# Kernel tuning notes

Hardware: AMD Instinct MI355X
Metric: run time of the kernel (lower is better)

Reference implementation:

```python
import jax, jax.numpy as jnp
import numpy as np

TAU = 0.5
EPS = 1e-6
RAY_STEPS = 128
N_SECANT = 8
STEPS_IN = 64
STEPS_OUT = 32
RADIUS = 1.0
ADA_START, ADA_END, ADA_DECAY = 2.0, 0.1, 1.5e-5
IT = 100000
DEPTH_NEAR = 0.0
DELTA = float(max(ADA_START * np.exp(-ADA_DECAY * IT), ADA_END))


def _occ_val(p, W1, b1, W2, b2):
    # occupancy probability minus tau (sign change = surface crossing)
    h = jax.nn.softplus(p @ W1 + b1)
    return jax.nn.sigmoid((h @ W2 + b2)[..., 0]) - TAU


def _rgb_alpha(p, v, W1, b1, W2, b2, Wc1, bc1, Wc2, bc2):
    alpha = _occ_val(p, W1, b1, W2, b2) + TAU
    f = jax.nn.relu(jnp.concatenate([p, v], -1) @ Wc1 + bc1)
    rgb = jax.nn.sigmoid(f @ Wc2 + bc2)
    return rgb, alpha


def _forward(pixels, camera_mat, world_mat, scale_mat, W1, b1, W2, b2, Wc1, bc1, Wc2, bc2):
    B, N, _ = pixels.shape
    # transform_to_world with all matrices inverted: p_world = S^-1 W^-1 C^-1 p_hom
    M = jnp.linalg.inv(scale_mat) @ jnp.linalg.inv(world_mat) @ jnp.linalg.inv(camera_mat)
    ones = jnp.ones((B, N, 1), pixels.dtype)
    p_h = jnp.concatenate([pixels, ones, ones], -1)  # (x, y, 1, 1) with depth 1
    pixels_world = jnp.einsum('bij,bnj->bni', M, p_h)[..., :3]
    origin = jnp.array([0.0, 0.0, 0.0, 1.0], pixels.dtype)
    cam0 = jnp.einsum('bij,j->bi', M, origin)[..., :3]                 # (B,3)
    camera_world = jnp.broadcast_to(cam0[:, None, :], (B, N, 3))
    ray = pixels_world - camera_world
    ray = ray / jnp.linalg.norm(ray, axis=-1, keepdims=True)

    # ---- sphere intersection ----
    rcd = jnp.einsum('bnd,bd->bn', ray, cam0)
    under = rcd ** 2 - (jnp.sum(cam0 ** 2, -1)[:, None] - RADIUS ** 2)
    mask_int = under > 0
    s = jnp.sqrt(jnp.where(mask_int, under, 1.0))                      # safe sqrt
    inters = jnp.stack([-s - rcd, s - rcd], -1)
    inters = jnp.where(mask_int[..., None], inters, 0.0)
    inters = jnp.maximum(inters, 0.0)                                  # (B,N,2)
    d_far = inters[..., 1]

    # ---- ray marching + secant root finding (no grad in original) ----
    t = jnp.linspace(0.0, 1.0, RAY_STEPS, dtype=pixels.dtype)
    d_prop = d_far[..., None] * t                                      # (B,N,S)
    p_prop = camera_world[:, :, None, :] + ray[:, :, None, :] * d_prop[..., None]
    val = _occ_val(p_prop, W1, b1, W2, b2)                             # (B,N,S)
    mask_0_free = val[..., 0] < 0
    sign = jnp.sign(val[..., :-1] * val[..., 1:])
    sign = jnp.concatenate([sign, jnp.ones_like(sign[..., :1])], -1)
    cost = sign * jnp.arange(RAY_STEPS, 0, -1, dtype=pixels.dtype)
    ind = jnp.argmin(cost, -1)
    mask_sc = jnp.min(cost, -1) < 0
    f_low = jnp.take_along_axis(val, ind[..., None], -1)[..., 0]
    mask = mask_sc & (f_low < 0) & mask_int & mask_0_free
    ind_hi = jnp.minimum(ind + 1, RAY_STEPS - 1)
    d_low = jnp.take_along_axis(d_prop, ind[..., None], -1)[..., 0]
    d_high = jnp.take_along_axis(d_prop, ind_hi[..., None], -1)[..., 0]
    f_high = jnp.take_along_axis(val, ind_hi[..., None], -1)[..., 0]

    def sec(f_l, f_h, d_l, d_h):
        den = f_h - f_l
        return jnp.where(jnp.abs(den) > 1e-12, -f_l * (d_h - d_l) / den + d_l, 0.5 * (d_l + d_h))

    def body(i, c):
        d_p, d_l, f_l, d_h, f_h = c
        f_m = _occ_val(camera_world + ray * d_p[..., None], W1, b1, W2, b2)
        low = f_m < 0
        d_l = jnp.where(low, d_p, d_l); f_l = jnp.where(low, f_m, f_l)
        d_h = jnp.where(low, d_h, d_p); f_h = jnp.where(low, f_h, f_m)
        return (sec(f_l, f_h, d_l, d_h), d_l, f_l, d_h, f_h)

    d_pred0 = sec(f_low, f_high, d_low, d_high)
    d_pred, _, _, _, _ = jax.lax.fori_loop(0, N_SECANT, body, (d_pred0, d_low, f_low, d_high, f_high))
    d_i = jnp.where(mask, d_pred, jnp.inf)
    d_i = jnp.where(mask_0_free, d_i, 0.0)
    d_i = jax.lax.stop_gradient(d_i)

    # ---- depth interval selection ----
    mask_zero = d_i == 0
    mask_pred = jnp.isfinite(d_i)
    dists = jnp.where(mask_pred, d_i, 1.0)
    dists = jnp.where(mask_zero, 0.0, dists)[0]                        # batch 1, as original
    obj_mask = (mask_pred & ~mask_zero)[0]                             # (N,)
    cam_f = camera_world.reshape(-1, 3)
    ray_f = ray.reshape(-1, 3)
    d_surf = inters.reshape(-1, 2)[:, 1]
    dnp = jnp.maximum(dists - DELTA, DEPTH_NEAR)
    dfp = jnp.minimum(dists + DELTA, d_surf)
    FULL = STEPS_IN + STEPS_OUT
    t_full = jnp.linspace(0.0, 1.0, FULL, dtype=pixels.dtype)
    d_bg = d_surf[:, None] * t_full                                    # depth_range[0] = 0
    t_in = jnp.linspace(0.0, 1.0, STEPS_IN, dtype=pixels.dtype)
    t_out = jnp.linspace(0.0, 1.0, STEPS_OUT, dtype=pixels.dtype)
    d_in = dnp[:, None] * (1.0 - t_in) + dfp[:, None] * t_in
    d_out = dnp[:, None] * t_out
    d_obj = jnp.sort(jnp.concatenate([d_out, d_in], -1), -1)
    d_all = jnp.where(obj_mask[:, None], d_obj, d_bg)                  # (N, FULL)

    # ---- shading + alpha compositing ----
    p_fg = cam_f[:, None, :] + ray_f[:, None, :] * d_all[..., None]    # (N,FULL,3)
    v_fg = jnp.broadcast_to(-ray_f[:, None, :], p_fg.shape)
    rgb, alpha = _rgb_alpha(p_fg, v_fg, W1, b1, W2, b2, Wc1, bc1, Wc2, bc2)
    trans = jnp.cumprod(jnp.concatenate([jnp.ones_like(alpha[:, :1]), 1.0 - alpha + EPS], -1), -1)[:, :-1]
    w = alpha * trans
    rgb_values = jnp.sum(w[..., None] * rgb, -2)
    return rgb_values.reshape(B, N, 3)


def setup_inputs() -> dict:
    key = jax.random.key(0)
    ks = jax.random.split(key, 8)
    B, N, H = 1, 4096, 128
    pixels = jax.random.uniform(ks[0], (B, N, 2), minval=-1.0, maxval=1.0, dtype=jnp.float32)
    camera_mat = jnp.broadcast_to(jnp.diag(jnp.array([2.0, 2.0, 1.0, 1.0], jnp.float32)), (B, 4, 4))
    world_mat = jnp.broadcast_to(jnp.array([[1, 0, 0, 0], [0, 1, 0, 0], [0, 0, 1, 2.0], [0, 0, 0, 1]], jnp.float32), (B, 4, 4))
    scale_mat = jnp.broadcast_to(jnp.eye(4, dtype=jnp.float32), (B, 4, 4))
    W1 = jax.random.normal(ks[1], (3, H), jnp.float32)
    b1 = 0.1 * jax.random.normal(ks[2], (H,), jnp.float32)
    W2 = 0.5 * jax.random.normal(ks[3], (H, 1), jnp.float32)
    b2 = jnp.zeros((1,), jnp.float32)
    Wc1 = 0.5 * jax.random.normal(ks[4], (6, H), jnp.float32)
    bc1 = jnp.zeros((H,), jnp.float32)
    Wc2 = 0.5 * jax.random.normal(ks[5], (H, 3), jnp.float32)
    bc2 = jnp.zeros((3,), jnp.float32)
    return dict(pixels=pixels, camera_mat=camera_mat, world_mat=world_mat, scale_mat=scale_mat,
                W1=W1, b1=b1, W2=W2, b2=b2, Wc1=Wc1, bc1=bc1, Wc2=Wc2, bc2=bc2)


def reference(pixels, camera_mat, world_mat, scale_mat, W1, b1, W2, b2, Wc1, bc1, Wc2, bc2):
    return _forward(pixels, camera_mat, world_mat, scale_mat, W1, b1, W2, b2, Wc1, bc1, Wc2, bc2)
```

## Files before the change

kernel.cpp:

```cpp
#include <hip/hip_runtime.h>
#include <math.h>


namespace {

constexpr int H_    = 128;
constexpr int RS    = 128;
constexpr int NSEC  = 8;
constexpr int SOUT_ = 32;
constexpr int SIN_  = 64;
constexpr int FULL_ = 96;
constexpr int RPB   = 4;
constexpr float EPSA   = 1e-6f;
constexpr float DELTA_ = 0.44626032029685964f;
constexpr float L2E    = 1.4426950408889634f;
constexpr float LN2    = 0.6931471805599453f;

typedef __attribute__((ext_vector_type(2))) float f2;

__device__ __forceinline__ f2 s2(float v) { return f2{v, v}; }

constexpr float PC0 =  0.5849625007211562f;
constexpr float PC1 =  0.4808983469629878f;
constexpr float PC2 = -0.0801497244938313f;
constexpr float PC3 =  0.0178110498875181f;
constexpr float PC4 = -0.0044527624718795f;
constexpr float PC5 =  0.0011873633258345f;
constexpr float PC6 = -0.0003298231460651f;

__device__ __forceinline__ f2 sp2p(f2 u) {
    f2 e;
    e.x = __builtin_amdgcn_exp2f(-fabsf(u.x));
    e.y = __builtin_amdgcn_exp2f(-fabsf(u.y));
    f2 t = e + e - 1.0f;
    f2 p = s2(PC6);
    p = __builtin_elementwise_fma(p, t, s2(PC5));
    p = __builtin_elementwise_fma(p, t, s2(PC4));
    p = __builtin_elementwise_fma(p, t, s2(PC3));
    p = __builtin_elementwise_fma(p, t, s2(PC2));
    p = __builtin_elementwise_fma(p, t, s2(PC1));
    p = __builtin_elementwise_fma(p, t, s2(PC0));
    return __builtin_elementwise_max(u, s2(0.0f)) + p;
}

__device__ __forceinline__ float sigmoid_fast(float x) {
    return __builtin_amdgcn_rcpf(1.0f + __expf(-x));
}
__device__ __forceinline__ float sgnf(float p) {
    return (p > 0.0f) ? 1.0f : ((p < 0.0f) ? -1.0f : 0.0f);
}
__device__ __forceinline__ float secant_step(float f_l, float f_h, float d_l, float d_h) {
    float den = f_h - f_l;
    if (fabsf(den) > 1e-12f) return -f_l * (d_h - d_l) / den + d_l;
    return 0.5f * (d_l + d_h);
}
__device__ __forceinline__ float2 ld2(const float* p) {
    return *reinterpret_cast<const float2*>(p);
}

__device__ void inv4(const float* m, float* o) {
    float inv[16];
    inv[0]  =  m[5]*m[10]*m[15] - m[5]*m[11]*m[14] - m[9]*m[6]*m[15] + m[9]*m[7]*m[14] + m[13]*m[6]*m[11] - m[13]*m[7]*m[10];
    inv[4]  = -m[4]*m[10]*m[15] + m[4]*m[11]*m[14] + m[8]*m[6]*m[15] - m[8]*m[7]*m[14] - m[12]*m[6]*m[11] + m[12]*m[7]*m[10];
    inv[8]  =  m[4]*m[9]*m[15]  - m[4]*m[11]*m[13] - m[8]*m[5]*m[15] + m[8]*m[7]*m[13] + m[12]*m[5]*m[11] - m[12]*m[7]*m[9];
    inv[12] = -m[4]*m[9]*m[14]  + m[4]*m[10]*m[13] + m[8]*m[5]*m[14] - m[8]*m[6]*m[13] - m[12]*m[5]*m[10] + m[12]*m[6]*m[9];
    inv[1]  = -m[1]*m[10]*m[15] + m[1]*m[11]*m[14] + m[9]*m[2]*m[15] - m[9]*m[3]*m[14] - m[13]*m[2]*m[11] + m[13]*m[3]*m[10];
    inv[5]  =  m[0]*m[10]*m[15] - m[0]*m[11]*m[14] - m[8]*m[2]*m[15] + m[8]*m[3]*m[14] + m[12]*m[2]*m[11] - m[12]*m[3]*m[10];
    inv[9]  = -m[0]*m[9]*m[15]  + m[0]*m[11]*m[13] + m[8]*m[1]*m[15] - m[8]*m[3]*m[13] - m[12]*m[1]*m[11] + m[12]*m[3]*m[9];
    inv[13] =  m[0]*m[9]*m[14]  - m[0]*m[10]*m[13] - m[8]*m[1]*m[14] + m[8]*m[2]*m[13] + m[12]*m[1]*m[10] - m[12]*m[2]*m[9];
    inv[2]  =  m[1]*m[6]*m[15]  - m[1]*m[7]*m[14]  - m[5]*m[2]*m[15] + m[5]*m[3]*m[14] + m[13]*m[2]*m[7]  - m[13]*m[3]*m[6];
    inv[6]  = -m[0]*m[6]*m[15]  + m[0]*m[7]*m[14]  + m[4]*m[2]*m[15] - m[4]*m[3]*m[14] - m[12]*m[2]*m[7]  + m[12]*m[3]*m[6];
    inv[10] =  m[0]*m[5]*m[15]  - m[0]*m[7]*m[13]  - m[4]*m[1]*m[15] + m[4]*m[3]*m[13] + m[12]*m[1]*m[7]  - m[12]*m[3]*m[5];
    inv[14] = -m[0]*m[5]*m[14]  + m[0]*m[6]*m[13]  + m[4]*m[1]*m[14] - m[4]*m[2]*m[13] - m[12]*m[1]*m[6]  + m[12]*m[2]*m[5];
    inv[3]  = -m[1]*m[6]*m[11]  + m[1]*m[7]*m[10]  + m[5]*m[2]*m[11] - m[5]*m[3]*m[10] - m[9]*m[2]*m[7]   + m[9]*m[3]*m[6];
    inv[7]  =  m[0]*m[6]*m[11]  - m[0]*m[7]*m[10]  - m[4]*m[2]*m[11] + m[4]*m[3]*m[10] + m[8]*m[2]*m[7]   - m[8]*m[3]*m[6];
    inv[11] = -m[0]*m[5]*m[11]  + m[0]*m[7]*m[9]   + m[4]*m[1]*m[11] - m[4]*m[3]*m[9]  - m[8]*m[1]*m[7]   + m[8]*m[3]*m[5];
    inv[15] =  m[0]*m[5]*m[10]  - m[0]*m[6]*m[9]   - m[4]*m[1]*m[10] + m[4]*m[2]*m[9]  + m[8]*m[1]*m[6]   - m[8]*m[2]*m[5];
    float det = m[0]*inv[0] + m[1]*inv[4] + m[2]*inv[8] + m[3]*inv[12];
    float idet = 1.0f / det;
    for (int i = 0; i < 16; i++) o[i] = inv[i] * idet;
}

__global__ __launch_bounds__(64 * RPB) void render_k(
    const float* __restrict__ pixels,
    const float* __restrict__ Cm, const float* __restrict__ Wm, const float* __restrict__ Sm,
    const float* __restrict__ W1, const float* __restrict__ b1,
    const float* __restrict__ W2, const float* __restrict__ b2,
    const float* __restrict__ Wc1, const float* __restrict__ bc1,
    const float* __restrict__ Wc2, const float* __restrict__ bc2,
    float* __restrict__ out, int N)
{
    const int tid  = threadIdx.x;
    const int lane = tid & 63;
    const int wid  = tid >> 6;
    const int r    = blockIdx.x * RPB + wid;
    const int rr   = (r < N) ? r : (N - 1);

    __shared__ float4 sP0[RPB][H_/2];
    __shared__ float4 sP1[RPB][H_/2];
    __shared__ float4 sP2[RPB][H_/2];
    __shared__ float4 sP3[RPB][H_/2];
    __shared__ f2     sW2[RPB][H_/2];
    __shared__ float  sInv[3][16];
    __shared__ float  sT[16], sM[16];

    const int u0 = 2 * lane;
    const float2 w1xv = ld2(W1 + u0);
    const float2 w1yv = ld2(W1 + H_ + u0);
    const float2 w1zv = ld2(W1 + 2*H_ + u0);
    const float2 b1v  = ld2(b1 + u0);
    const float2 w2v  = ld2(W2 + u0);
    const float2 q0v  = ld2(Wc1 + u0);
    const float2 q1v  = ld2(Wc1 + H_ + u0);
    const float2 q2v  = ld2(Wc1 + 2*H_ + u0);
    const float2 q3v  = ld2(Wc1 + 3*H_ + u0);
    const float2 q4v  = ld2(Wc1 + 4*H_ + u0);
    const float2 q5v  = ld2(Wc1 + 5*H_ + u0);
    const float2 bc1v = ld2(bc1 + u0);
    const float2 wc2a = ld2(Wc2 + 3*u0);
    const float2 wc2b = ld2(Wc2 + 3*u0 + 2);
    const float2 wc2c = ld2(Wc2 + 3*u0 + 4);
    const float b2v  = b2[0];
    const float bc20 = bc2[0], bc21 = bc2[1], bc22 = bc2[2];

    if (wid == 0) {
        const float* mm = (lane == 0) ? Cm : ((lane == 1) ? Wm : Sm);
        float o[16];
        inv4(mm, o);
        if (lane < 3)
            for (int k = 0; k < 16; k++) sInv[lane][k] = o[k];
    }
    __syncthreads();
    if (wid == 0 && lane < 16) {
        int row = lane >> 2, col = lane & 3;
        float s = 0.0f;
        for (int k = 0; k < 4; k++) s += sInv[1][row*4 + k] * sInv[0][k*4 + col];
        sT[lane] = s;
    }
    __syncthreads();
    if (wid == 0 && lane < 16) {
        int row = lane >> 2, col = lane & 3;
        float s = 0.0f;
        for (int k = 0; k < 4; k++) s += sInv[2][row*4 + k] * sT[k*4 + col];
        sM[lane] = s;
    }
    __syncthreads();

    float cx, cy, cz, rx, ry, rz, dfar;
    int mint;
    {
        const float px_ = pixels[2*rr], py_ = pixels[2*rr + 1];
        float cam[3], dir[3];
        for (int i = 0; i < 3; i++) {
            cam[i] = sM[4*i + 3];
            float pw = sM[4*i + 0]*px_ + sM[4*i + 1]*py_ + sM[4*i + 2] + sM[4*i + 3];
            dir[i] = pw - cam[i];
        }
        float nrm = sqrtf(dir[0]*dir[0] + dir[1]*dir[1] + dir[2]*dir[2]);
        rx = dir[0]/nrm; ry = dir[1]/nrm; rz = dir[2]/nrm;
        cx = cam[0]; cy = cam[1]; cz = cam[2];
        float rcd = rx*cx + ry*cy + rz*cz;
        float cc  = cx*cx + cy*cy + cz*cz;
        float under = rcd*rcd - (cc - 1.0f);
        mint = under > 0.0f;
        float s = sqrtf(mint ? under : 1.0f);
        dfar = mint ? fmaxf(s - rcd, 0.0f) : 0.0f;
    }

    float a2k[2], c2k[2], w2k[2];
    float cCr[2], w0r[2], w1r[2], w2r[2];
    {
        a2k[0] = (w1xv.x*rx + w1yv.x*ry + w1zv.x*rz) * L2E;
        a2k[1] = (w1xv.y*rx + w1yv.y*ry + w1zv.y*rz) * L2E;
        c2k[0] = (w1xv.x*cx + w1yv.x*cy + w1zv.x*cz + b1v.x) * L2E;
        c2k[1] = (w1xv.y*cx + w1yv.y*cy + w1zv.y*cz + b1v.y) * L2E;
        w2k[0] = w2v.x * LN2;
        w2k[1] = w2v.y * LN2;
        float aC0 = q0v.x*rx + q1v.x*ry + q2v.x*rz;
        float aC1 = q0v.y*rx + q1v.y*ry + q2v.y*rz;
        cCr[0] = q0v.x*cx + q1v.x*cy + q2v.x*cz + bc1v.x - (q3v.x*rx + q4v.x*ry + q5v.x*rz);
        cCr[1] = q0v.y*cx + q1v.y*cy + q2v.y*cz + bc1v.y - (q3v.y*rx + q4v.y*ry + q5v.y*rz);
        w0r[0] = wc2a.x; w1r[0] = wc2a.y; w2r[0] = wc2b.x;
        w0r[1] = wc2b.y; w1r[1] = wc2c.x; w2r[1] = wc2c.y;
        sP0[wid][lane] = float4{a2k[0], a2k[1], c2k[0], c2k[1]};
        sP1[wid][lane] = float4{w2k[0], w2k[1], aC0, aC1};
        sP2[wid][lane] = float4{cCr[0], cCr[1], w0r[0], w0r[1]};
        sP3[wid][lane] = float4{w1r[0], w1r[1], w2r[0], w2r[1]};
        sW2[wid][lane] = f2{w2k[0], w2k[1]};
    }
    __syncthreads();

    float alpha0, r0c, g0c, b0c;
    float alpha1, r1c, g1c, b1c;

    if (dfar == 0.0f) {
        f2 sp = sp2p(f2{c2k[0], c2k[1]});
        float part = sp.x*w2k[0] + sp.y*w2k[1];
        f2 ff = __builtin_elementwise_max(f2{cCr[0], cCr[1]}, s2(0.0f));
        float A0 = ff.x*w0r[0] + ff.y*w0r[1];
        float A1 = ff.x*w1r[0] + ff.y*w1r[1];
        float A2 = ff.x*w2r[0] + ff.y*w2r[1];
#pragma unroll
        for (int off = 32; off; off >>= 1) {
            part += __shfl_xor(part, off, 64);
            A0   += __shfl_xor(A0,   off, 64);
            A1   += __shfl_xor(A1,   off, 64);
            A2   += __shfl_xor(A2,   off, 64);
        }
        alpha0 = sigmoid_fast(part + b2v);
        r0c = sigmoid_fast(A0 + bc20);
        g0c = sigmoid_fast(A1 + bc21);
        b0c = sigmoid_fast(A2 + bc22);
        alpha1 = alpha0; r1c = r0c; g1c = g0c; b1c = b0c;
    } else {
        const float inv127 = 1.0f / (RS - 1);

        float l0;
        {
            f2 sp = sp2p(f2{c2k[0], c2k[1]});
            float part = sp.x*w2k[0] + sp.y*w2k[1];
#pragma unroll
            for (int off = 32; off; off >>= 1) part += __shfl_xor(part, off, 64);
            l0 = part + b2v;
        }

        float d_i;
        if (l0 >= 0.0f) {
            d_i = 0.0f;
        } else {
            auto march_logit = [&](float dsmp) -> float {
                const f2 dd = s2(dsmp);
                f2 acc = s2(0.0f);
#pragma unroll 4
                for (int j2 = 0; j2 < H_/2; j2++) {
                    float4 q0 = sP0[wid][j2];
                    f2 wv = sW2[wid][j2];
                    f2 u = __builtin_elementwise_fma(f2{q0.x, q0.y}, dd, f2{q0.z, q0.w});
                    acc = __builtin_elementwise_fma(sp2p(u), wv, acc);
                }
                return acc.x + acc.y + b2v;
            };

            float lA = march_logit(dfar * ((float)lane * inv127));
            float va = sigmoid_fast(lA) - 0.5f;
            float van = __shfl_down(va, 1, 64);
            float ca = (lane < 63) ? sgnf(va * van) * (float)(RS - lane) : 1.0f;
            float cmin = ca; int ind = lane;
#pragma unroll
            for (int off = 32; off; off >>= 1) {
                float c2 = __shfl_xor(cmin, off, 64);
                int   i2 = __shfl_xor(ind,  off, 64);
                if (c2 < cmin || (c2 == cmin && i2 < ind)) { cmin = c2; ind = i2; }
            }
            int crossed = cmin < 0.0f;
            float f_low = 0.0f, f_high = 0.0f;
            if (crossed) {
                f_low  = __shfl(va, ind, 64);
                f_high = __shfl(va, ind + 1, 64);
            } else {
                float lB = march_logit(dfar * ((float)(lane + 64) * inv127));
                float vb = sigmoid_fast(lB) - 0.5f;
                float v63 = __shfl(va, 63, 64);
                float v64 = __shfl(vb, 0, 64);
                if (v63 * v64 < 0.0f) {
                    crossed = 1; ind = 63;
                    f_low = v63; f_high = v64;
                } else {
                    float vbn = __shfl_down(vb, 1, 64);
                    float cb = (lane < 63) ? sgnf(vb * vbn) * (float)(64 - lane) : 1.0f;
                    float cminb = cb; int indl = lane;
#pragma unroll
                    for (int off = 32; off; off >>= 1) {
                        float c2 = __shfl_xor(cminb, off, 64);
                        int   i2 = __shfl_xor(indl,  off, 64);
                        if (c2 < cminb || (c2 == cminb && i2 < indl)) { cminb = c2; indl = i2; }
                    }
                    if (cminb < 0.0f) {
                        crossed = 1; ind = 64 + indl;
                        f_low  = __shfl(vb, indl, 64);
                        f_high = __shfl(vb, indl + 1, 64);
                    }
                }
            }

            const int msk = crossed && (f_low < 0.0f) && mint;
            if (msk) {
                float d_l = dfar * ((float)ind * inv127);
                float d_h = dfar * ((float)(ind + 1) * inv127);
                float f_l = f_low, f_h = f_high;
                float d_p = secant_step(f_l, f_h, d_l, d_h);
                for (int it = 0; it < NSEC; it++) {
                    f2 u2 = __builtin_elementwise_fma(f2{a2k[0], a2k[1]}, s2(d_p),
                                                      f2{c2k[0], c2k[1]});
                    f2 sp = sp2p(u2);
                    float part = sp.x*w2k[0] + sp.y*w2k[1];
#pragma unroll
                    for (int off = 32; off; off >>= 1) part += __shfl_xor(part, off, 64);
                    float fm = sigmoid_fast(part + b2v) - 0.5f;
                    bool low = fm < 0.0f;
                    d_l = low ? d_p : d_l;  f_l = low ? fm : f_l;
                    d_h = low ? d_h : d_p;  f_h = low ? f_h : fm;
                    d_p = secant_step(f_l, f_h, d_l, d_h);
                }
                d_i = d_p;
            } else {
                d_i = INFINITY;
            }
        }

        const int mask_zero = (d_i == 0.0f);
        const int mask_pred = isfinite(d_i);
        float dists = mask_pred ? d_i : 1.0f;
        if (mask_zero) dists = 0.0f;
        const int obj = mask_pred && !mask_zero;
        const float dnp = fmaxf(dists - DELTA_, 0.0f);
        const float dfp = fminf(dists + DELTA_, dfar);

        auto sample_d = [&](int s) -> float {
            if (obj) {
                if (s < SOUT_) return dnp * ((float)s * (1.0f / (SOUT_ - 1)));
                float u = (float)(s - SOUT_) * (1.0f / (SIN_ - 1));
                return dnp * (1.0f - u) + dfp * u;
            }
            return dfar * ((float)s * (1.0f / (FULL_ - 1)));
        };

        {
            const f2 dd = s2(sample_d(lane));
            f2 SO = s2(0.0f), A0 = s2(0.0f), A1 = s2(0.0f), A2 = s2(0.0f);
#pragma unroll 4
            for (int j2 = 0; j2 < H_/2; j2++) {
                float4 q0 = sP0[wid][j2];
                float4 q1 = sP1[wid][j2];
                float4 q2 = sP2[wid][j2];
                float4 q3 = sP3[wid][j2];
                f2 u = __builtin_elementwise_fma(f2{q0.x, q0.y}, dd, f2{q0.z, q0.w});
                SO = __builtin_elementwise_fma(sp2p(u), f2{q1.x, q1.y}, SO);
                f2 f = __builtin_elementwise_max(
                           __builtin_elementwise_fma(f2{q1.z, q1.w}, dd, f2{q2.x, q2.y}),
                           s2(0.0f));
                A0 = __builtin_elementwise_fma(f, f2{q2.z, q2.w}, A0);
                A1 = __builtin_elementwise_fma(f, f2{q3.x, q3.y}, A1);
                A2 = __builtin_elementwise_fma(f, f2{q3.z, q3.w}, A2);
            }
            alpha0 = sigmoid_fast(SO.x + SO.y + b2v);
            r0c = sigmoid_fast(A0.x + A0.y + bc20);
            g0c = sigmoid_fast(A1.x + A1.y + bc21);
            b0c = sigmoid_fast(A2.x + A2.y + bc22);
        }

        {
            const int s1 = 64 + (lane & 31);
            const int jb = (lane >> 5) * (H_/4);
            const f2 dd = s2(sample_d(s1));
            f2 SO = s2(0.0f), A0 = s2(0.0f), A1 = s2(0.0f), A2 = s2(0.0f);
#pragma unroll 4
            for (int j2 = jb; j2 < jb + H_/4; j2++) {
                float4 q0 = sP0[wid][j2];
                float4 q1 = sP1[wid][j2];
                float4 q2 = sP2[wid][j2];
                float4 q3 = sP3[wid][j2];
                f2 u = __builtin_elementwise_fma(f2{q0.x, q0.y}, dd, f2{q0.z, q0.w});
                SO = __builtin_elementwise_fma(sp2p(u), f2{q1.x, q1.y}, SO);
                f2 f = __builtin_elementwise_max(
                           __builtin_elementwise_fma(f2{q1.z, q1.w}, dd, f2{q2.x, q2.y}),
                           s2(0.0f));
                A0 = __builtin_elementwise_fma(f, f2{q2.z, q2.w}, A0);
                A1 = __builtin_elementwise_fma(f, f2{q3.x, q3.y}, A1);
                A2 = __builtin_elementwise_fma(f, f2{q3.z, q3.w}, A2);
            }
            float SOs = SO.x + SO.y, A0s = A0.x + A0.y;
            float A1s = A1.x + A1.y, A2s = A2.x + A2.y;
            SOs += __shfl_xor(SOs, 32, 64);
            A0s += __shfl_xor(A0s, 32, 64);
            A1s += __shfl_xor(A1s, 32, 64);
            A2s += __shfl_xor(A2s, 32, 64);
            alpha1 = sigmoid_fast(SOs + b2v);
            r1c = sigmoid_fast(A0s + bc20);
            g1c = sigmoid_fast(A1s + bc21);
            b1c = sigmoid_fast(A2s + bc22);
        }
    }

    {
        float mA = 1.0f - alpha0 + EPSA;
        float p = mA;
#pragma unroll
        for (int off = 1; off < 64; off <<= 1) {
            float v = __shfl_up(p, off, 64);
            if (lane >= off) p *= v;
        }
        float TexA = __shfl_up(p, 1, 64);
        if (lane == 0) TexA = 1.0f;
        float TA = __shfl(p, 63, 64);
        float wA = alpha0 * TexA;

        float mB = (lane < 32) ? (1.0f - alpha1 + EPSA) : 1.0f;
        float pb = mB;
#pragma unroll
        for (int off = 1; off < 32; off <<= 1) {
            float v = __shfl_up(pb, off, 64);
            if (lane >= off) pb *= v;
        }
        float TexB = __shfl_up(pb, 1, 64);
        if (lane == 0) TexB = 1.0f;
        float wB = (lane < 32) ? alpha1 * TexB * TA : 0.0f;

        float s0 = wA*r0c + wB*r1c;
        float s1 = wA*g0c + wB*g1c;
        float s2v = wA*b0c + wB*b1c;
#pragma unroll
        for (int off = 32; off; off >>= 1) {
            s0  += __shfl_xor(s0,  off, 64);
            s1  += __shfl_xor(s1,  off, 64);
            s2v += __shfl_xor(s2v, off, 64);
        }
        if (lane == 0 && r < N) {
            out[3*r + 0] = s0;
            out[3*r + 1] = s1;
            out[3*r + 2] = s2v;
        }
    }
}

}

extern "C" void kernel_launch(void* const* d_in, const int* in_sizes, int n_in,
                              void* d_out, int out_size, void* d_ws, size_t ws_size,
                              hipStream_t stream) {
    const float* pixels = (const float*)d_in[0];
    const float* Cm  = (const float*)d_in[1];
    const float* Wm  = (const float*)d_in[2];
    const float* Sm  = (const float*)d_in[3];
    const float* W1  = (const float*)d_in[4];
    const float* b1  = (const float*)d_in[5];
    const float* W2  = (const float*)d_in[6];
    const float* b2  = (const float*)d_in[7];
    const float* Wc1 = (const float*)d_in[8];
    const float* bc1 = (const float*)d_in[9];
    const float* Wc2 = (const float*)d_in[10];
    const float* bc2 = (const float*)d_in[11];
    float* out = (float*)d_out;

    const int N = in_sizes[0] / 2;
    const int nblk = (N + RPB - 1) / RPB;
    hipLaunchKernelGGL(render_k, dim3(nblk), dim3(64 * RPB), 0, stream,
                       pixels, Cm, Wm, Sm, W1, b1, W2, b2, Wc1, bc1, Wc2, bc2, out, N);
}
```

Before: 98.98 us.

## Use one-wave blocks, Estrin softplus polynomial, prefetched LDS loops, logit-space sign tests

```diff
diff --git a/kernel.cpp b/kernel.cpp
--- a/kernel.cpp
+++ b/kernel.cpp
@@ -10,7 +10,6 @@
 constexpr int SOUT_ = 32;
 constexpr int SIN_  = 64;
 constexpr int FULL_ = 96;
-constexpr int RPB   = 4;
 constexpr float EPSA   = 1e-6f;
 constexpr float DELTA_ = 0.44626032029685964f;
 constexpr float L2E    = 1.4426950408889634f;
@@ -32,14 +31,15 @@
     f2 e;
     e.x = __builtin_amdgcn_exp2f(-fabsf(u.x));
     e.y = __builtin_amdgcn_exp2f(-fabsf(u.y));
-    f2 t = e + e - 1.0f;
-    f2 p = s2(PC6);
-    p = __builtin_elementwise_fma(p, t, s2(PC5));
-    p = __builtin_elementwise_fma(p, t, s2(PC4));
-    p = __builtin_elementwise_fma(p, t, s2(PC3));
-    p = __builtin_elementwise_fma(p, t, s2(PC2));
-    p = __builtin_elementwise_fma(p, t, s2(PC1));
-    p = __builtin_elementwise_fma(p, t, s2(PC0));
+    f2 t  = e + e - 1.0f;
+    f2 t2 = t * t;
+    f2 t4 = t2 * t2;
+    f2 A = __builtin_elementwise_fma(t, s2(PC1), s2(PC0));
+    f2 B = __builtin_elementwise_fma(t, s2(PC3), s2(PC2));
+    f2 C = __builtin_elementwise_fma(t, s2(PC5), s2(PC4));
+    f2 E = __builtin_elementwise_fma(t2, B, A);
+    f2 F = __builtin_elementwise_fma(t2, s2(PC6), C);
+    f2 p = __builtin_elementwise_fma(t4, F, E);
     return __builtin_elementwise_max(u, s2(0.0f)) + p;
 }
 
@@ -81,7 +81,7 @@
     for (int i = 0; i < 16; i++) o[i] = inv[i] * idet;
 }
 
-__global__ __launch_bounds__(64 * RPB) void render_k(
+__global__ __launch_bounds__(64) void render_k(
     const float* __restrict__ pixels,
     const float* __restrict__ Cm, const float* __restrict__ Wm, const float* __restrict__ Sm,
     const float* __restrict__ W1, const float* __restrict__ b1,
@@ -90,19 +90,17 @@
     const float* __restrict__ Wc2, const float* __restrict__ bc2,
     float* __restrict__ out, int N)
 {
-    const int tid  = threadIdx.x;
-    const int lane = tid & 63;
-    const int wid  = tid >> 6;
-    const int r    = blockIdx.x * RPB + wid;
-    const int rr   = (r < N) ? r : (N - 1);
-
-    __shared__ float4 sP0[RPB][H_/2];
-    __shared__ float4 sP1[RPB][H_/2];
-    __shared__ float4 sP2[RPB][H_/2];
-    __shared__ float4 sP3[RPB][H_/2];
-    __shared__ f2     sW2[RPB][H_/2];
+    const int lane = threadIdx.x;
+    const int r    = blockIdx.x;
+
+    __shared__ float4 sP0[H_/2];
+    __shared__ float4 sP1[H_/2];
+    __shared__ float4 sP2[H_/2];
+    __shared__ float4 sP3[H_/2];
+    __shared__ f2     sW2[H_/2];
     __shared__ float  sInv[3][16];
     __shared__ float  sT[16], sM[16];
+    __shared__ float  sPad[16];
 
     const int u0 = 2 * lane;
     const float2 w1xv = ld2(W1 + u0);
@@ -123,7 +121,7 @@
     const float b2v  = b2[0];
     const float bc20 = bc2[0], bc21 = bc2[1], bc22 = bc2[2];
 
-    if (wid == 0) {
+    {
         const float* mm = (lane == 0) ? Cm : ((lane == 1) ? Wm : Sm);
         float o[16];
         inv4(mm, o);
@@ -131,14 +129,14 @@
             for (int k = 0; k < 16; k++) sInv[lane][k] = o[k];
     }
     __syncthreads();
-    if (wid == 0 && lane < 16) {
+    if (lane < 16) {
         int row = lane >> 2, col = lane & 3;
         float s = 0.0f;
         for (int k = 0; k < 4; k++) s += sInv[1][row*4 + k] * sInv[0][k*4 + col];
         sT[lane] = s;
     }
     __syncthreads();
-    if (wid == 0 && lane < 16) {
+    if (lane < 16) {
         int row = lane >> 2, col = lane & 3;
         float s = 0.0f;
         for (int k = 0; k < 4; k++) s += sInv[2][row*4 + k] * sT[k*4 + col];
@@ -149,7 +147,7 @@
     float cx, cy, cz, rx, ry, rz, dfar;
     int mint;
     {
-        const float px_ = pixels[2*rr], py_ = pixels[2*rr + 1];
+        const float px_ = pixels[2*r], py_ = pixels[2*r + 1];
         float cam[3], dir[3];
         for (int i = 0; i < 3; i++) {
             cam[i] = sM[4*i + 3];
@@ -182,11 +180,12 @@
         cCr[1] = q0v.y*cx + q1v.y*cy + q2v.y*cz + bc1v.y - (q3v.y*rx + q4v.y*ry + q5v.y*rz);
         w0r[0] = wc2a.x; w1r[0] = wc2a.y; w2r[0] = wc2b.x;
         w0r[1] = wc2b.y; w1r[1] = wc2c.x; w2r[1] = wc2c.y;
-        sP0[wid][lane] = float4{a2k[0], a2k[1], c2k[0], c2k[1]};
-        sP1[wid][lane] = float4{w2k[0], w2k[1], aC0, aC1};
-        sP2[wid][lane] = float4{cCr[0], cCr[1], w0r[0], w0r[1]};
-        sP3[wid][lane] = float4{w1r[0], w1r[1], w2r[0], w2r[1]};
-        sW2[wid][lane] = f2{w2k[0], w2k[1]};
+        sP0[lane] = float4{a2k[0], a2k[1], c2k[0], c2k[1]};
+        sP1[lane] = float4{w2k[0], w2k[1], aC0, aC1};
+        sP2[lane] = float4{cCr[0], cCr[1], w0r[0], w0r[1]};
+        sP3[lane] = float4{w1r[0], w1r[1], w2r[0], w2r[1]};
+        sW2[lane] = f2{w2k[0], w2k[1]};
+        if (lane < 16) sPad[lane] = 0.0f;
     }
     __syncthreads();
 
@@ -230,21 +229,33 @@
         } else {
             auto march_logit = [&](float dsmp) -> float {
                 const f2 dd = s2(dsmp);
-                f2 acc = s2(0.0f);
-#pragma unroll 4
-                for (int j2 = 0; j2 < H_/2; j2++) {
-                    float4 q0 = sP0[wid][j2];
-                    f2 wv = sW2[wid][j2];
-                    f2 u = __builtin_elementwise_fma(f2{q0.x, q0.y}, dd, f2{q0.z, q0.w});
-                    acc = __builtin_elementwise_fma(sp2p(u), wv, acc);
-                }
+                f2 acc0 = s2(0.0f), acc1 = s2(0.0f);
+                float4 nb[4]; f2 nw[4];
+#pragma unroll
+                for (int k = 0; k < 4; ++k) { nb[k] = sP0[k]; nw[k] = sW2[k]; }
+                for (int g = 0; g < H_/8; ++g) {
+                    float4 cb[4]; f2 cw[4];
+#pragma unroll
+                    for (int k = 0; k < 4; ++k) { cb[k] = nb[k]; cw[k] = nw[k]; }
+                    const int base = (g + 1) * 4;
+#pragma unroll
+                    for (int k = 0; k < 4; ++k) { nb[k] = sP0[base + k]; nw[k] = sW2[base + k]; }
+#pragma unroll
+                    for (int k = 0; k < 4; ++k) {
+                        f2 u = __builtin_elementwise_fma(f2{cb[k].x, cb[k].y}, dd,
+                                                         f2{cb[k].z, cb[k].w});
+                        f2 s = sp2p(u);
+                        if (k & 1) acc1 = __builtin_elementwise_fma(s, cw[k], acc1);
+                        else       acc0 = __builtin_elementwise_fma(s, cw[k], acc0);
+                    }
+                }
+                f2 acc = acc0 + acc1;
                 return acc.x + acc.y + b2v;
             };
 
             float lA = march_logit(dfar * ((float)lane * inv127));
-            float va = sigmoid_fast(lA) - 0.5f;
-            float van = __shfl_down(va, 1, 64);
-            float ca = (lane < 63) ? sgnf(va * van) * (float)(RS - lane) : 1.0f;
+            float lan = __shfl_down(lA, 1, 64);
+            float ca = (lane < 63) ? sgnf(lA * lan) * (float)(RS - lane) : 1.0f;
             float cmin = ca; int ind = lane;
 #pragma unroll
             for (int off = 32; off; off >>= 1) {
@@ -253,21 +264,20 @@
                 if (c2 < cmin || (c2 == cmin && i2 < ind)) { cmin = c2; ind = i2; }
             }
             int crossed = cmin < 0.0f;
-            float f_low = 0.0f, f_high = 0.0f;
+            float ll = 0.0f, lh = 0.0f;
             if (crossed) {
-                f_low  = __shfl(va, ind, 64);
-                f_high = __shfl(va, ind + 1, 64);
+                ll = __shfl(lA, ind, 64);
+                lh = __shfl(lA, ind + 1, 64);
             } else {
                 float lB = march_logit(dfar * ((float)(lane + 64) * inv127));
-                float vb = sigmoid_fast(lB) - 0.5f;
-                float v63 = __shfl(va, 63, 64);
-                float v64 = __shfl(vb, 0, 64);
-                if (v63 * v64 < 0.0f) {
+                float l63 = __shfl(lA, 63, 64);
+                float l64 = __shfl(lB, 0, 64);
+                if (l63 * l64 < 0.0f) {
                     crossed = 1; ind = 63;
-                    f_low = v63; f_high = v64;
+                    ll = l63; lh = l64;
                 } else {
-                    float vbn = __shfl_down(vb, 1, 64);
-                    float cb = (lane < 63) ? sgnf(vb * vbn) * (float)(64 - lane) : 1.0f;
+                    float lbn = __shfl_down(lB, 1, 64);
+                    float cb = (lane < 63) ? sgnf(lB * lbn) * (float)(64 - lane) : 1.0f;
                     float cminb = cb; int indl = lane;
 #pragma unroll
                     for (int off = 32; off; off >>= 1) {
@@ -277,14 +287,16 @@
                     }
                     if (cminb < 0.0f) {
                         crossed = 1; ind = 64 + indl;
-                        f_low  = __shfl(vb, indl, 64);
-                        f_high = __shfl(vb, indl + 1, 64);
+                        ll = __shfl(lB, indl, 64);
+                        lh = __shfl(lB, indl + 1, 64);
                     }
                 }
             }
 
-            const int msk = crossed && (f_low < 0.0f) && mint;
+            const int msk = crossed && (ll < 0.0f) && mint;
             if (msk) {
+                float f_low  = sigmoid_fast(ll) - 0.5f;
+                float f_high = sigmoid_fast(lh) - 0.5f;
                 float d_l = dfar * ((float)ind * inv127);
                 float d_h = dfar * ((float)(ind + 1) * inv127);
                 float f_l = f_low, f_h = f_high;
@@ -325,52 +337,60 @@
             return dfar * ((float)s * (1.0f / (FULL_ - 1)));
         };
 
+        auto shade = [&](int jb, int cnt, float dsmp,
+                         float& SOo, float& A0o, float& A1o, float& A2o) {
+            const f2 dd = s2(dsmp);
+            f2 SO = s2(0.0f), A0 = s2(0.0f), A1 = s2(0.0f), A2 = s2(0.0f);
+            float4 n0[2], n1[2], n2[2], n3[2];
+#pragma unroll
+            for (int k = 0; k < 2; ++k) {
+                n0[k] = sP0[jb + k]; n1[k] = sP1[jb + k];
+                n2[k] = sP2[jb + k]; n3[k] = sP3[jb + k];
+            }
+            for (int g = 0; g < cnt/2; ++g) {
+                float4 c0[2], c1[2], c2q[2], c3[2];
+#pragma unroll
+                for (int k = 0; k < 2; ++k) {
+                    c0[k] = n0[k]; c1[k] = n1[k]; c2q[k] = n2[k]; c3[k] = n3[k];
+                }
+                const int base = jb + (g + 1) * 2;
+#pragma unroll
+                for (int k = 0; k < 2; ++k) {
+                    n0[k] = sP0[base + k]; n1[k] = sP1[base + k];
+                    n2[k] = sP2[base + k]; n3[k] = sP3[base + k];
+                }
+#pragma unroll
+                for (int k = 0; k < 2; ++k) {
+                    f2 u = __builtin_elementwise_fma(f2{c0[k].x, c0[k].y}, dd,
+                                                     f2{c0[k].z, c0[k].w});
+                    SO = __builtin_elementwise_fma(sp2p(u), f2{c1[k].x, c1[k].y}, SO);
+                    f2 f = __builtin_elementwise_max(
+                               __builtin_elementwise_fma(f2{c1[k].z, c1[k].w}, dd,
+                                                         f2{c2q[k].x, c2q[k].y}),
+                               s2(0.0f));
+                    A0 = __builtin_elementwise_fma(f, f2{c2q[k].z, c2q[k].w}, A0);
+                    A1 = __builtin_elementwise_fma(f, f2{c3[k].x, c3[k].y}, A1);
+                    A2 = __builtin_elementwise_fma(f, f2{c3[k].z, c3[k].w}, A2);
+                }
+            }
+            SOo = SO.x + SO.y; A0o = A0.x + A0.y;
+            A1o = A1.x + A1.y; A2o = A2.x + A2.y;
+        };
+
         {
-            const f2 dd = s2(sample_d(lane));
-            f2 SO = s2(0.0f), A0 = s2(0.0f), A1 = s2(0.0f), A2 = s2(0.0f);
-#pragma unroll 4
-            for (int j2 = 0; j2 < H_/2; j2++) {
-                float4 q0 = sP0[wid][j2];
-                float4 q1 = sP1[wid][j2];
-                float4 q2 = sP2[wid][j2];
-                float4 q3 = sP3[wid][j2];
-                f2 u = __builtin_elementwise_fma(f2{q0.x, q0.y}, dd, f2{q0.z, q0.w});
-                SO = __builtin_elementwise_fma(sp2p(u), f2{q1.x, q1.y}, SO);
-                f2 f = __builtin_elementwise_max(
-                           __builtin_elementwise_fma(f2{q1.z, q1.w}, dd, f2{q2.x, q2.y}),
-                           s2(0.0f));
-                A0 = __builtin_elementwise_fma(f, f2{q2.z, q2.w}, A0);
-                A1 = __builtin_elementwise_fma(f, f2{q3.x, q3.y}, A1);
-                A2 = __builtin_elementwise_fma(f, f2{q3.z, q3.w}, A2);
-            }
-            alpha0 = sigmoid_fast(SO.x + SO.y + b2v);
-            r0c = sigmoid_fast(A0.x + A0.y + bc20);
-            g0c = sigmoid_fast(A1.x + A1.y + bc21);
-            b0c = sigmoid_fast(A2.x + A2.y + bc22);
+            float SOs, A0s, A1s, A2s;
+            shade(0, H_/2, sample_d(lane), SOs, A0s, A1s, A2s);
+            alpha0 = sigmoid_fast(SOs + b2v);
+            r0c = sigmoid_fast(A0s + bc20);
+            g0c = sigmoid_fast(A1s + bc21);
+            b0c = sigmoid_fast(A2s + bc22);
         }
 
         {
             const int s1 = 64 + (lane & 31);
             const int jb = (lane >> 5) * (H_/4);
-            const f2 dd = s2(sample_d(s1));
-            f2 SO = s2(0.0f), A0 = s2(0.0f), A1 = s2(0.0f), A2 = s2(0.0f);
-#pragma unroll 4
-            for (int j2 = jb; j2 < jb + H_/4; j2++) {
-                float4 q0 = sP0[wid][j2];
-                float4 q1 = sP1[wid][j2];
-                float4 q2 = sP2[wid][j2];
-                float4 q3 = sP3[wid][j2];
-                f2 u = __builtin_elementwise_fma(f2{q0.x, q0.y}, dd, f2{q0.z, q0.w});
-                SO = __builtin_elementwise_fma(sp2p(u), f2{q1.x, q1.y}, SO);
-                f2 f = __builtin_elementwise_max(
-                           __builtin_elementwise_fma(f2{q1.z, q1.w}, dd, f2{q2.x, q2.y}),
-                           s2(0.0f));
-                A0 = __builtin_elementwise_fma(f, f2{q2.z, q2.w}, A0);
-                A1 = __builtin_elementwise_fma(f, f2{q3.x, q3.y}, A1);
-                A2 = __builtin_elementwise_fma(f, f2{q3.z, q3.w}, A2);
-            }
-            float SOs = SO.x + SO.y, A0s = A0.x + A0.y;
-            float A1s = A1.x + A1.y, A2s = A2.x + A2.y;
+            float SOs, A0s, A1s, A2s;
+            shade(jb, H_/4, sample_d(s1), SOs, A0s, A1s, A2s);
             SOs += __shfl_xor(SOs, 32, 64);
             A0s += __shfl_xor(A0s, 32, 64);
             A1s += __shfl_xor(A1s, 32, 64);
@@ -415,7 +435,7 @@
             s1  += __shfl_xor(s1,  off, 64);
             s2v += __shfl_xor(s2v, off, 64);
         }
-        if (lane == 0 && r < N) {
+        if (lane == 0) {
             out[3*r + 0] = s0;
             out[3*r + 1] = s1;
             out[3*r + 2] = s2v;
@@ -443,7 +463,6 @@
     float* out = (float*)d_out;
 
     const int N = in_sizes[0] / 2;
-    const int nblk = (N + RPB - 1) / RPB;
-    hipLaunchKernelGGL(render_k, dim3(nblk), dim3(64 * RPB), 0, stream,
+    hipLaunchKernelGGL(render_k, dim3(N), dim3(64), 0, stream,
                        pixels, Cm, Wm, Sm, W1, b1, W2, b2, Wc1, bc1, Wc2, bc2, out, N);
 }
```

Measured after the change: 105.7 us. 6.8% more time.
